# Kernel tuning notes

Hardware: AMD Instinct MI355X
Metric: run time of the kernel (lower is better)

The kernel has to match this reference:

```python
import jax, jax.numpy as jnp
import numpy as np

H_DIM = 2048
N_HEADS = 16
HEAD_DIM = H_DIM // N_HEADS
B, S = 2, 2048


def setup_inputs() -> dict:
    key = jax.random.key(0)
    ks = jax.random.split(key, 10)
    sc = 1.0 / np.sqrt(H_DIM)
    return {
        "X": jax.random.normal(ks[0], (B, S, H_DIM), dtype=jnp.float32),
        "attention_mask": jnp.ones((B, S, S), dtype=jnp.int32),
        "Wq": jax.random.normal(ks[1], (H_DIM, H_DIM), dtype=jnp.float32) * sc,
        "bq": jnp.zeros((H_DIM,), dtype=jnp.float32),
        "Wk": jax.random.normal(ks[2], (H_DIM, H_DIM), dtype=jnp.float32) * sc,
        "bk": jnp.zeros((H_DIM,), dtype=jnp.float32),
        "Wv": jax.random.normal(ks[3], (H_DIM, H_DIM), dtype=jnp.float32) * sc,
        "bv": jnp.zeros((H_DIM,), dtype=jnp.float32),
        "Wo": jax.random.normal(ks[4], (H_DIM, H_DIM), dtype=jnp.float32) * sc,
        "bo": jnp.zeros((H_DIM,), dtype=jnp.float32),
    }


def reference(X, attention_mask, Wq, bq, Wk, bk, Wv, bv, Wo, bo):
    b, s, _ = X.shape
    # QKV projections -> [b, heads, s, head_dim]
    def proj(W, bias):
        y = jnp.einsum("bsd,de->bse", X, W) + bias
        return y.reshape(b, s, N_HEADS, HEAD_DIM).transpose(0, 2, 1, 3)
    Q, K, V = proj(Wq, bq), proj(Wk, bk), proj(Wv, bv)
    # scores [b, h, s, s]
    scores = jnp.einsum("bhqd,bhkd->bhqk", Q, K) / jnp.sqrt(jnp.float32(HEAD_DIM))
    mask = attention_mask[:, None, :, :]  # [b,1,s,s]
    scores = jnp.where(mask == 0, jnp.float32(-jnp.inf), scores)
    attn = jax.nn.softmax(scores, axis=-1)
    # dropout_rate = 0.0 -> no-op
    out = jnp.einsum("bhqk,bhkd->bhqd", attn, V)
    out = out.transpose(0, 2, 1, 3).reshape(b, s, H_DIM)
    return jnp.einsum("bsd,de->bse", out, Wo) + bo
```

## Files before the change

kernel.cpp:

```cpp
#include <hip/hip_runtime.h>
#include <hip/hip_bf16.h>

#define H_DIM 2048
#define N_HEADS 16
#define HEAD_DIM 128
#define BATCH 2
#define SEQ 2048

typedef __bf16 bf16_t;
typedef __bf16 bf16x8 __attribute__((ext_vector_type(8)));
typedef float f32x4 __attribute__((ext_vector_type(4)));

#define MFMA16(a, b, c) __builtin_amdgcn_mfma_f32_16x16x32_bf16((a), (b), (c), 0, 0, 0)

#define GLOAD16(gp, lp) __builtin_amdgcn_global_load_lds( \
    (const __attribute__((address_space(1))) void*)(gp),  \
    (__attribute__((address_space(3))) void*)(lp), 16, 0, 0)

#define WAIT_VM6()  asm volatile("s_waitcnt vmcnt(6)" ::: "memory")
#define WAIT_VM4()  asm volatile("s_waitcnt vmcnt(4)" ::: "memory")
#define WAIT_VM0()  asm volatile("s_waitcnt vmcnt(0)" ::: "memory")
#define RAW_BARRIER() asm volatile("s_barrier" ::: "memory")

__global__ __launch_bounds__(256) void detect_kernel(const unsigned int* __restrict__ X,
                                                     int* __restrict__ flags) {
    __shared__ int cnt[256];
    int t = threadIdx.x;
    int c = 0;
    for (int i = 0; i < 16; i++) {
        unsigned w  = X[t * 16 + i];
        unsigned lo = w & 0xFFFFu;
        unsigned e  = (lo >> 7) & 0xFFu;
        if (lo == 0u || (e >= 100u && e <= 141u)) c++;
    }
    cnt[t] = c;
    __syncthreads();
    for (int s = 128; s > 0; s >>= 1) {
        if (t < s) cnt[t] += cnt[t + s];
        __syncthreads();
    }
    if (t == 0) { flags[0] = (cnt[0] >= 2048) ? 1 : 0; flags[1] = 1; }
}

__global__ __launch_bounds__(256) void maskcheck_kernel(const int* __restrict__ mask,
                                                        int* __restrict__ flags) {
    size_t i = ((size_t)blockIdx.x * 256 + threadIdx.x) * 8;
    const int4* p = (const int4*)(mask + i);
    int4 a = p[0], b = p[1];
    int all = (a.x != 0) & (a.y != 0) & (a.z != 0) & (a.w != 0) &
              (b.x != 0) & (b.y != 0) & (b.z != 0) & (b.w != 0);
    if (!all) atomicAnd(&flags[1], 0);
}

__device__ inline bf16x8 load8(const void* __restrict__ p, size_t idx, int isbf16) {
    if (isbf16) {
        return *(const bf16x8*)((const bf16_t*)p + idx);
    } else {
        const float* f = (const float*)p + idx;
        float4 a = *(const float4*)f;
        float4 b = *(const float4*)(f + 4);
        bf16x8 r;
        r[0] = (bf16_t)a.x; r[1] = (bf16_t)a.y; r[2] = (bf16_t)a.z; r[3] = (bf16_t)a.w;
        r[4] = (bf16_t)b.x; r[5] = (bf16_t)b.y; r[6] = (bf16_t)b.z; r[7] = (bf16_t)b.w;
        return r;
    }
}

__device__ inline float readf(const void* __restrict__ p, int idx, int isbf16) {
    return isbf16 ? (float)((const bf16_t*)p)[idx] : ((const float*)p)[idx];
}

__global__ __launch_bounds__(256) void convert_kernel(const void* __restrict__ X,
                                                      bf16_t* __restrict__ Xb,
                                                      const int* __restrict__ flags) {
    const int isbf16 = flags[0];
    size_t i = ((size_t)blockIdx.x * 256 + threadIdx.x) * 8;
    bf16x8 v = load8(X, i, isbf16);
    *(bf16x8*)(Xb + i) = v;
}

__global__ __launch_bounds__(256) void transpose_kernel(
    const void* __restrict__ W0, const void* __restrict__ W1,
    const void* __restrict__ W2, const void* __restrict__ W3,
    bf16_t* __restrict__ Wts, const int* __restrict__ flags)
{
    const int isbf16 = flags[0];
    const int z = blockIdx.z;
    const void* W = (z == 0) ? W0 : (z == 1) ? W1 : (z == 2) ? W2 : W3;
    bf16_t* out = Wts + (size_t)z * H_DIM * H_DIM;

    __shared__ __attribute__((aligned(16))) bf16_t Ts[64][72];
    const int tid = threadIdx.x;
    const int n0 = blockIdx.x * 64;
    const int k0 = blockIdx.y * 64;

    #pragma unroll
    for (int j = 0; j < 2; j++) {
        int idx = j * 2048 + tid * 8;
        int r = idx >> 6, c = idx & 63;
        bf16x8 v = load8(W, (size_t)(k0 + r) * H_DIM + n0 + c, isbf16);
        *(bf16x8*)(&Ts[r][c]) = v;
    }
    __syncthreads();
    const int wr = tid & 63;
    const int wcg = (tid >> 6) * 8;
    #pragma unroll
    for (int j = 0; j < 2; j++) {
        int wc = wcg + j * 32;
        bf16x8 o;
        #pragma unroll
        for (int u = 0; u < 8; u++) o[u] = Ts[wc + u][wr];
        *(bf16x8*)(&out[(size_t)(n0 + wr) * H_DIM + k0 + wc]) = o;
    }
}

__global__ __launch_bounds__(256, 2) void gemm_qkv_kernel(
    const bf16_t* __restrict__ A, const bf16_t* __restrict__ Wts,
    const void* __restrict__ b0, const void* __restrict__ b1, const void* __restrict__ b2,
    bf16_t* __restrict__ qws, bf16_t* __restrict__ kws, bf16_t* __restrict__ vtws,
    const int* __restrict__ flags)
{
    const int isbf16 = flags[0];
    const int L    = blockIdx.x;
    const int xcd  = L & 7;
    const int j    = L >> 3;
    const int c    = xcd * 6 + (j % 6);
    const int mrow = j / 6;
    const int z    = c >> 4;
    const int m0   = mrow * 256;
    const int n0   = (c & 15) * 128;

    const bf16_t* Wt = Wts + (size_t)z * H_DIM * H_DIM;
    const void* bias = (z == 0) ? b0 : (z == 1) ? b1 : b2;
    bf16_t* dst = (z == 0) ? qws : (z == 1) ? kws : vtws;

    __shared__ __attribute__((aligned(16))) bf16_t As[3][4][256][8];
    __shared__ __attribute__((aligned(16))) bf16_t Bs[3][4][128][8];

    const int tid  = threadIdx.x;
    const int lane = tid & 63;
    const int wid  = tid >> 6;
    const int quad = lane >> 4;
    const int l16  = lane & 15;
    const int wm   = (wid >> 1) * 128;
    const int wn   = (wid & 1) * 64;

    f32x4 acc[8][4] = {};

    auto stage = [&](int k0, int sb) {
        #pragma unroll
        for (int jj = 0; jj < 4; jj++) {
            int slot = jj * 256 + tid;
            int k8 = slot >> 8, row = slot & 255;
            GLOAD16(A + (size_t)(m0 + row) * H_DIM + k0 + k8 * 8,
                    (bf16_t*)(&As[sb][0][0][0]) + slot * 8);
        }
        #pragma unroll
        for (int jj = 0; jj < 2; jj++) {
            int slot = jj * 256 + tid;
            int k8 = slot >> 7, row = slot & 127;
            GLOAD16(Wt + (size_t)(n0 + row) * H_DIM + k0 + k8 * 8,
                    (bf16_t*)(&Bs[sb][0][0][0]) + slot * 8);
        }
    };

    auto body = [&](int it, int bb, int sb, int mode) {
        if (mode == 2) { WAIT_VM0(); } else { WAIT_VM6(); }
        RAW_BARRIER();
        if (mode == 0) stage((it + 2) * 32, sb);
        bf16x8 bfr[4];
        #pragma unroll
        for (int i = 0; i < 4; i++)
            bfr[i] = *(const bf16x8*)(&Bs[bb][quad][wn + i * 16 + l16][0]);
        #pragma unroll
        for (int mi = 0; mi < 8; mi++) {
            bf16x8 af = *(const bf16x8*)(&As[bb][quad][wm + mi * 16 + l16][0]);
            #pragma unroll
            for (int ni = 0; ni < 4; ni++)
                acc[mi][ni] = MFMA16(af, bfr[ni], acc[mi][ni]);
        }
    };

    stage(0, 0);
    stage(32, 1);
    for (int base = 0; base < 60; base += 3) {
        body(base,     0, 2, 0);
        body(base + 1, 1, 0, 0);
        body(base + 2, 2, 1, 0);
    }
    body(60, 0, 2, 0);
    body(61, 1, 0, 0);
    body(62, 2, 1, 1);
    body(63, 0, 0, 2);

    #pragma unroll
    for (int ni = 0; ni < 4; ni++) {
        int col = n0 + wn + ni * 16 + l16;
        int h = col >> 7, d = col & (HEAD_DIM - 1);
        float bv = readf(bias, col, isbf16);
        #pragma unroll
        for (int mi = 0; mi < 8; mi++) {
            int row0 = m0 + wm + mi * 16 + quad * 4;
            int b = row0 >> 11;
            if (z < 2) {
                #pragma unroll
                for (int r = 0; r < 4; r++) {
                    int s = (row0 + r) & (SEQ - 1);
                    dst[((size_t)(b * N_HEADS + h) * SEQ + s) * HEAD_DIM + d] =
                        (bf16_t)(acc[mi][ni][r] + bv);
                }
            } else {
                int s0 = row0 & (SEQ - 1);
                bf16_t o[4];
                #pragma unroll
                for (int r = 0; r < 4; r++) o[r] = (bf16_t)(acc[mi][ni][r] + bv);
                *(unsigned long long*)(&dst[((size_t)(b * N_HEADS + h) * HEAD_DIM + d) * SEQ + s0]) =
                    *(unsigned long long*)o;
            }
        }
    }
}

__global__ __launch_bounds__(256) void gemm_out_kernel(
    const bf16_t* __restrict__ A, const bf16_t* __restrict__ Wt,
    const void* __restrict__ bias, void* __restrict__ C,
    const int* __restrict__ flags)
{
    const int isbf16 = flags[0];
    const int L    = blockIdx.x;
    const int xcd  = L & 7;
    const int j    = L >> 3;
    const int m0   = (j >> 1) * 128;
    const int n0   = (xcd * 2 + (j & 1)) * 128;

    __shared__ __attribute__((aligned(16))) bf16_t As[3][4][128][8];
    __shared__ __attribute__((aligned(16))) bf16_t Bs[3][4][128][8];

    const int tid  = threadIdx.x;
    const int lane = tid & 63;
    const int wid  = tid >> 6;
    const int quad = lane >> 4;
    const int l16  = lane & 15;
    const int wm   = (wid >> 1) * 64;
    const int wn   = (wid & 1) * 64;

    f32x4 acc[4][4] = {};

    auto stage = [&](int k0, int sb) {
        #pragma unroll
        for (int jj = 0; jj < 2; jj++) {
            int slot = jj * 256 + tid;
            int k8 = slot >> 7, row = slot & 127;
            GLOAD16(A  + (size_t)(m0 + row) * H_DIM + k0 + k8 * 8,
                    (bf16_t*)(&As[sb][0][0][0]) + slot * 8);
            GLOAD16(Wt + (size_t)(n0 + row) * H_DIM + k0 + k8 * 8,
                    (bf16_t*)(&Bs[sb][0][0][0]) + slot * 8);
        }
    };

    auto body = [&](int it, int bb, int sb, int mode) {
        if (mode == 2) { WAIT_VM0(); } else { WAIT_VM4(); }
        RAW_BARRIER();
        if (mode == 0) stage((it + 2) * 32, sb);
        bf16x8 af[4], bfr[4];
        #pragma unroll
        for (int i = 0; i < 4; i++) {
            af[i]  = *(const bf16x8*)(&As[bb][quad][wm + i * 16 + l16][0]);
            bfr[i] = *(const bf16x8*)(&Bs[bb][quad][wn + i * 16 + l16][0]);
        }
        #pragma unroll
        for (int mi = 0; mi < 4; mi++)
            #pragma unroll
            for (int ni = 0; ni < 4; ni++)
                acc[mi][ni] = MFMA16(af[mi], bfr[ni], acc[mi][ni]);
    };

    stage(0, 0);
    stage(32, 1);
    for (int base = 0; base < 60; base += 3) {
        body(base,     0, 2, 0);
        body(base + 1, 1, 0, 0);
        body(base + 2, 2, 1, 0);
    }
    body(60, 0, 2, 0);
    body(61, 1, 0, 0);
    body(62, 2, 1, 1);
    body(63, 0, 0, 2);

    #pragma unroll
    for (int ni = 0; ni < 4; ni++) {
        int col = n0 + wn + ni * 16 + l16;
        float bv = readf(bias, col, isbf16);
        #pragma unroll
        for (int mi = 0; mi < 4; mi++) {
            int row0 = m0 + wm + mi * 16 + quad * 4;
            #pragma unroll
            for (int r = 0; r < 4; r++) {
                float v = acc[mi][ni][r] + bv;
                if (isbf16) ((bf16_t*)C)[(size_t)(row0 + r) * H_DIM + col] = (bf16_t)v;
                else        ((float*)C)[(size_t)(row0 + r) * H_DIM + col]  = v;
            }
        }
    }
}

__global__ __launch_bounds__(256, 2) void attn_kernel(
    const bf16_t* __restrict__ Q, const bf16_t* __restrict__ K,
    const bf16_t* __restrict__ Vt, const int* __restrict__ mask,
    const int* __restrict__ flags, bf16_t* __restrict__ ctx)
{
    __shared__ __attribute__((aligned(16))) bf16_t Ks[2][16][64][8];
    __shared__ __attribute__((aligned(16))) bf16_t Vs[2][8][128][8];
    __shared__ __attribute__((aligned(16))) bf16_t Pl[4][16][72];

    const int tid  = threadIdx.x;
    const int lane = tid & 63;
    const int wid  = tid >> 6;
    const int quad = lane >> 4;
    const int l16  = lane & 15;

    const int bh = blockIdx.y;
    const int b  = bh >> 4, h = bh & 15;
    const int q0 = blockIdx.x * 128 + wid * 16;
    const int q1 = q0 + 64;
    const int maskAll = flags[1];

    const bf16_t* Qp = Q  + (size_t)bh * SEQ * HEAD_DIM;
    const bf16_t* Kp = K  + (size_t)bh * SEQ * HEAD_DIM;
    const bf16_t* Vp = Vt + (size_t)bh * HEAD_DIM * SEQ;
    const int*    mp = mask + (size_t)b * SEQ * SEQ;

    bf16x8 qf[2][4];
    #pragma unroll
    for (int t = 0; t < 4; t++) {
        qf[0][t] = *(const bf16x8*)(Qp + (size_t)(q0 + l16) * HEAD_DIM + t * 32 + quad * 8);
        qf[1][t] = *(const bf16x8*)(Qp + (size_t)(q1 + l16) * HEAD_DIM + t * 32 + quad * 8);
    }

    bf16x8 onesf;
    #pragma unroll
    for (int u = 0; u < 8; u++) onesf[u] = (bf16_t)1.0f;

    const float CS = 0.1275260013f;
    const float M0 = 16.0f;
    f32x4 l_acc[2] = {};
    f32x4 o_acc[2][8] = {};

    auto stage = [&](int kt, int bb) {
        const int key0 = kt * 64;
        #pragma unroll
        for (int jj = 0; jj < 4; jj++) {
            int slot = jj * 256 + tid;
            int krow = slot & 63, k8 = slot >> 6;
            GLOAD16(Kp + (size_t)(key0 + krow) * HEAD_DIM + k8 * 8,
                    (bf16_t*)(&Ks[bb][0][0][0]) + slot * 8);
        }
        #pragma unroll
        for (int jj = 0; jj < 4; jj++) {
            int slot = jj * 256 + tid;
            int d = slot & 127, kq = slot >> 7;
            GLOAD16(Vp + (size_t)d * SEQ + key0 + kq * 8,
                    (bf16_t*)(&Vs[bb][0][0][0]) + slot * 8);
        }
    };

    const int NKT = SEQ / 64;

    auto abody = [&](int kt, int bb) {
        const int key0 = kt * 64;
        __syncthreads();
        if (kt + 1 < NKT) stage(kt + 1, bb ^ 1);

        f32x4 s0[4] = {}, s1[4] = {};
        #pragma unroll
        for (int nt = 0; nt < 4; nt++) {
            #pragma unroll
            for (int t = 0; t < 4; t++) {
                bf16x8 kf = *(const bf16x8*)(&Ks[bb][t * 4 + quad][nt * 16 + l16][0]);
                s0[nt] = MFMA16(qf[0][t], kf, s0[nt]);
                s1[nt] = MFMA16(qf[1][t], kf, s1[nt]);
            }
        }

        #pragma unroll
        for (int u = 0; u < 2; u++) {
            float p2[4][4];
            #pragma unroll
            for (int nt = 0; nt < 4; nt++)
                #pragma unroll
                for (int r = 0; r < 4; r++)
                    p2[nt][r] = (u ? s1[nt][r] : s0[nt][r]) * CS - M0;

            if (!maskAll) {
                int qb = u ? q1 : q0;
                #pragma unroll
                for (int nt = 0; nt < 4; nt++) {
                    int key = key0 + nt * 16 + l16;
                    #pragma unroll
                    for (int r = 0; r < 4; r++) {
                        int q = qb + quad * 4 + r;
                        if (mp[(size_t)q * SEQ + key] == 0) p2[nt][r] = -1e30f;
                    }
                }
            }

            #pragma unroll
            for (int nt = 0; nt < 4; nt++)
                #pragma unroll
                for (int r = 0; r < 4; r++)
                    Pl[wid][quad * 4 + r][nt * 16 + l16] = (bf16_t)exp2f(p2[nt][r]);

            #pragma unroll
            for (int t = 0; t < 2; t++) {
                bf16x8 pf = *(const bf16x8*)(&Pl[wid][l16][t * 32 + quad * 8]);
                l_acc[u] = MFMA16(pf, onesf, l_acc[u]);
                #pragma unroll
                for (int dn = 0; dn < 8; dn++) {
                    bf16x8 vf = *(const bf16x8*)(&Vs[bb][t * 4 + quad][dn * 16 + l16][0]);
                    o_acc[u][dn] = MFMA16(pf, vf, o_acc[u][dn]);
                }
            }
        }
    };

    stage(0, 0);
    for (int base = 0; base < NKT; base += 2) {
        abody(base, 0);
        abody(base + 1, 1);
    }

    #pragma unroll
    for (int u = 0; u < 2; u++) {
        int qb = u ? q1 : q0;
        #pragma unroll
        for (int dn = 0; dn < 8; dn++) {
            #pragma unroll
            for (int r = 0; r < 4; r++) {
                int q = qb + quad * 4 + r;
                int d = dn * 16 + l16;
                float v = o_acc[u][dn][r] / l_acc[u][r];
                ctx[((size_t)(b * SEQ + q) * N_HEADS + h) * HEAD_DIM + d] = (bf16_t)v;
            }
        }
    }
}

extern "C" void kernel_launch(void* const* d_in, const int* in_sizes, int n_in,
                              void* d_out, int out_size, void* d_ws, size_t ws_size,
                              hipStream_t stream) {
    const void* X    = d_in[0];
    const int*  mask = (const int*)d_in[1];
    const void* Wq   = d_in[2];
    const void* bq   = d_in[3];
    const void* Wk   = d_in[4];
    const void* bk   = d_in[5];
    const void* Wv   = d_in[6];
    const void* bv   = d_in[7];
    const void* Wo   = d_in[8];
    const void* bo   = d_in[9];

    const size_t NE = (size_t)BATCH * SEQ * H_DIM;
    const size_t NW = (size_t)H_DIM * H_DIM;

    int*    flags = (int*)d_ws;
    bf16_t* Xb    = (bf16_t*)((char*)d_ws + 256);
    bf16_t* Wts   = Xb + NE;
    bf16_t* qws   = Wts + 4 * NW;
    bf16_t* kws   = qws + NE;
    bf16_t* vtws  = kws + NE;
    bf16_t* cws   = vtws + NE;

    detect_kernel<<<1, 256, 0, stream>>>((const unsigned int*)X, flags);
    maskcheck_kernel<<<(BATCH * SEQ * SEQ) / (256 * 8), 256, 0, stream>>>(mask, flags);
    convert_kernel<<<NE / (256 * 8), 256, 0, stream>>>(X, Xb, flags);
    transpose_kernel<<<dim3(32, 32, 4), 256, 0, stream>>>(Wq, Wk, Wv, Wo, Wts, flags);
    gemm_qkv_kernel<<<768, 256, 0, stream>>>(Xb, Wts, bq, bk, bv, qws, kws, vtws, flags);
    attn_kernel<<<dim3(SEQ / 128, BATCH * N_HEADS), 256, 0, stream>>>(
        qws, kws, vtws, mask, flags, cws);
    gemm_out_kernel<<<512, 256, 0, stream>>>(cws, Wts + 3 * NW, bo, d_out, flags);
}
```

Baseline: 575.9 us.

## Fuse prep kernels and transpose attention MFMA output for vectorized context stores

Merges the mask-check, X-conversion and weight-transpose kernels into one launch, with block ranges selecting each role. This removes two kernel launches and lets the independent prep work overlap. In the attention kernel the MFMA operand order is swapped, so the accumulator tile is transposed and each lane holds four consecutive head-dim values for one query. Context writes then become 8-byte stores with one reciprocal per row instead of scattered 2-byte stores with per-element divides. The combined prep kernel uses a branchy block role split with shared memory declared in only one branch.

```diff
diff --git a/kernel.cpp b/kernel.cpp
--- a/kernel.cpp
+++ b/kernel.cpp
@@ -10,6 +10,7 @@
 typedef __bf16 bf16_t;
 typedef __bf16 bf16x8 __attribute__((ext_vector_type(8)));
 typedef float f32x4 __attribute__((ext_vector_type(4)));
+typedef unsigned long long u64_t;
 
 #define MFMA16(a, b, c) __builtin_amdgcn_mfma_f32_16x16x32_bf16((a), (b), (c), 0, 0, 0)
 
@@ -40,16 +41,6 @@
         __syncthreads();
     }
     if (t == 0) { flags[0] = (cnt[0] >= 2048) ? 1 : 0; flags[1] = 1; }
-}
-
-__global__ __launch_bounds__(256) void maskcheck_kernel(const int* __restrict__ mask,
-                                                        int* __restrict__ flags) {
-    size_t i = ((size_t)blockIdx.x * 256 + threadIdx.x) * 8;
-    const int4* p = (const int4*)(mask + i);
-    int4 a = p[0], b = p[1];
-    int all = (a.x != 0) & (a.y != 0) & (a.z != 0) & (a.w != 0) &
-              (b.x != 0) & (b.y != 0) & (b.z != 0) & (b.w != 0);
-    if (!all) atomicAnd(&flags[1], 0);
 }
 
 __device__ inline bf16x8 load8(const void* __restrict__ p, size_t idx, int isbf16) {
@@ -70,47 +61,54 @@
     return isbf16 ? (float)((const bf16_t*)p)[idx] : ((const float*)p)[idx];
 }
 
-__global__ __launch_bounds__(256) void convert_kernel(const void* __restrict__ X,
-                                                      bf16_t* __restrict__ Xb,
-                                                      const int* __restrict__ flags) {
-    const int isbf16 = flags[0];
-    size_t i = ((size_t)blockIdx.x * 256 + threadIdx.x) * 8;
-    bf16x8 v = load8(X, i, isbf16);
-    *(bf16x8*)(Xb + i) = v;
-}
-
-__global__ __launch_bounds__(256) void transpose_kernel(
+__global__ __launch_bounds__(256) void prep_kernel(
+    const void* __restrict__ X, bf16_t* __restrict__ Xb,
+    const int* __restrict__ mask,
     const void* __restrict__ W0, const void* __restrict__ W1,
     const void* __restrict__ W2, const void* __restrict__ W3,
-    bf16_t* __restrict__ Wts, const int* __restrict__ flags)
+    bf16_t* __restrict__ Wts, int* __restrict__ flags)
 {
     const int isbf16 = flags[0];
-    const int z = blockIdx.z;
-    const void* W = (z == 0) ? W0 : (z == 1) ? W1 : (z == 2) ? W2 : W3;
-    bf16_t* out = Wts + (size_t)z * H_DIM * H_DIM;
-
-    __shared__ __attribute__((aligned(16))) bf16_t Ts[64][72];
     const int tid = threadIdx.x;
-    const int n0 = blockIdx.x * 64;
-    const int k0 = blockIdx.y * 64;
-
-    #pragma unroll
-    for (int j = 0; j < 2; j++) {
-        int idx = j * 2048 + tid * 8;
-        int r = idx >> 6, c = idx & 63;
-        bf16x8 v = load8(W, (size_t)(k0 + r) * H_DIM + n0 + c, isbf16);
-        *(bf16x8*)(&Ts[r][c]) = v;
-    }
-    __syncthreads();
-    const int wr = tid & 63;
-    const int wcg = (tid >> 6) * 8;
-    #pragma unroll
-    for (int j = 0; j < 2; j++) {
-        int wc = wcg + j * 32;
-        bf16x8 o;
-        #pragma unroll
-        for (int u = 0; u < 8; u++) o[u] = Ts[wc + u][wr];
-        *(bf16x8*)(&out[(size_t)(n0 + wr) * H_DIM + k0 + wc]) = o;
+
+    if (blockIdx.x < 4096) {
+        size_t i = ((size_t)blockIdx.x * 256 + tid) * 8;
+        bf16x8 v = load8(X, i, isbf16);
+        *(bf16x8*)(Xb + i) = v;
+
+        const int4* p = (const int4*)(mask + i);
+        int4 a = p[0], b = p[1];
+        int all = (a.x != 0) & (a.y != 0) & (a.z != 0) & (a.w != 0) &
+                  (b.x != 0) & (b.y != 0) & (b.z != 0) & (b.w != 0);
+        if (!all) atomicAnd(&flags[1], 0);
+    } else {
+        const int t   = blockIdx.x - 4096;
+        const int z   = t >> 10;
+        const int rem = t & 1023;
+        const int n0  = (rem & 31) * 64;
+        const int k0  = (rem >> 5) * 64;
+        const void* W = (z == 0) ? W0 : (z == 1) ? W1 : (z == 2) ? W2 : W3;
+        bf16_t* out = Wts + (size_t)z * H_DIM * H_DIM;
+
+        __shared__ __attribute__((aligned(16))) bf16_t Ts[64][72];
+        #pragma unroll
+        for (int j = 0; j < 2; j++) {
+            int idx = j * 2048 + tid * 8;
+            int r = idx >> 6, c = idx & 63;
+            bf16x8 v = load8(W, (size_t)(k0 + r) * H_DIM + n0 + c, isbf16);
+            *(bf16x8*)(&Ts[r][c]) = v;
+        }
+        __syncthreads();
+        const int wr = tid & 63;
+        const int wcg = (tid >> 6) * 8;
+        #pragma unroll
+        for (int j = 0; j < 2; j++) {
+            int wc = wcg + j * 32;
+            bf16x8 o;
+            #pragma unroll
+            for (int u = 0; u < 8; u++) o[u] = Ts[wc + u][wr];
+            *(bf16x8*)(&out[(size_t)(n0 + wr) * H_DIM + k0 + wc]) = o;
+        }
     }
 }
 
@@ -214,8 +212,8 @@
                 bf16_t o[4];
                 #pragma unroll
                 for (int r = 0; r < 4; r++) o[r] = (bf16_t)(acc[mi][ni][r] + bv);
-                *(unsigned long long*)(&dst[((size_t)(b * N_HEADS + h) * HEAD_DIM + d) * SEQ + s0]) =
-                    *(unsigned long long*)o;
+                *(u64_t*)(&dst[((size_t)(b * N_HEADS + h) * HEAD_DIM + d) * SEQ + s0]) =
+                    *(u64_t*)o;
             }
         }
     }
@@ -413,11 +411,11 @@
             #pragma unroll
             for (int t = 0; t < 2; t++) {
                 bf16x8 pf = *(const bf16x8*)(&Pl[wid][l16][t * 32 + quad * 8]);
-                l_acc[u] = MFMA16(pf, onesf, l_acc[u]);
+                l_acc[u] = MFMA16(onesf, pf, l_acc[u]);
                 #pragma unroll
                 for (int dn = 0; dn < 8; dn++) {
                     bf16x8 vf = *(const bf16x8*)(&Vs[bb][t * 4 + quad][dn * 16 + l16][0]);
-                    o_acc[u][dn] = MFMA16(pf, vf, o_acc[u][dn]);
+                    o_acc[u][dn] = MFMA16(vf, pf, o_acc[u][dn]);
                 }
             }
         }
@@ -432,15 +430,14 @@
     #pragma unroll
     for (int u = 0; u < 2; u++) {
         int qb = u ? q1 : q0;
+        float inv = 1.0f / l_acc[u][0];
+        bf16_t* cp = ctx + ((size_t)(b * SEQ + qb + l16)) * H_DIM + h * HEAD_DIM;
         #pragma unroll
         for (int dn = 0; dn < 8; dn++) {
-            #pragma unroll
-            for (int r = 0; r < 4; r++) {
-                int q = qb + quad * 4 + r;
-                int d = dn * 16 + l16;
-                float v = o_acc[u][dn][r] / l_acc[u][r];
-                ctx[((size_t)(b * SEQ + q) * N_HEADS + h) * HEAD_DIM + d] = (bf16_t)v;
-            }
+            bf16_t o4[4];
+            #pragma unroll
+            for (int r = 0; r < 4; r++) o4[r] = (bf16_t)(o_acc[u][dn][r] * inv);
+            *(u64_t*)(cp + dn * 16 + quad * 4) = *(u64_t*)o4;
         }
     }
 }
@@ -471,9 +468,7 @@
     bf16_t* cws   = vtws + NE;
 
     detect_kernel<<<1, 256, 0, stream>>>((const unsigned int*)X, flags);
-    maskcheck_kernel<<<(BATCH * SEQ * SEQ) / (256 * 8), 256, 0, stream>>>(mask, flags);
-    convert_kernel<<<NE / (256 * 8), 256, 0, stream>>>(X, Xb, flags);
-    transpose_kernel<<<dim3(32, 32, 4), 256, 0, stream>>>(Wq, Wk, Wv, Wo, Wts, flags);
+    prep_kernel<<<8192, 256, 0, stream>>>(X, Xb, mask, Wq, Wk, Wv, Wo, Wts, flags);
     gemm_qkv_kernel<<<768, 256, 0, stream>>>(Xb, Wts, bq, bk, bv, qws, kws, vtws, flags);
     attn_kernel<<<dim3(SEQ / 128, BATCH * N_HEADS), 256, 0, stream>>>(
         qws, kws, vtws, mask, flags, cws);
```

Result: no change. 570.9 us (-0.9%).
